# Optimization experiments

Measured on AMD Instinct MI355X. Metric: run time of the kernel, lower is better.

The kernel has to match this reference:

```python
import jax, jax.numpy as jnp
import numpy as np

SCORE_THR = 0.05
IOU_THR = 0.5
MAX_PER_IMG = 100
PRE_NMS_K = 2048  # fixed candidate budget for jit-compatible NMS
NUM_CLASSES = 80
MEANS = jnp.array([0.0, 0.0, 0.0, 0.0], jnp.float32)
STDS = jnp.array([0.1, 0.1, 0.2, 0.2], jnp.float32)
WH_RATIO_CLIP = 16.0 / 1000.0


def setup_inputs() -> dict:
    key = jax.random.key(0)
    B, N, C = 4, 8192, NUM_CLASSES
    H, W = 800, 1333
    k1, k2, k3, k4, k5, k6 = jax.random.split(key, 6)
    class_outs = jax.random.normal(k1, (B * N, C + 1), jnp.float32)
    regression_outs = jax.random.normal(k2, (B * N, C * 4), jnp.float32) * 0.5
    x1 = jax.random.uniform(k3, (B, N), minval=0.0, maxval=W * 0.8)
    y1 = jax.random.uniform(k4, (B, N), minval=0.0, maxval=H * 0.8)
    w = jax.random.uniform(k5, (B, N), minval=8.0, maxval=W * 0.2)
    h = jax.random.uniform(k6, (B, N), minval=8.0, maxval=H * 0.2)
    boxes = jnp.stack([x1, y1, jnp.minimum(x1 + w, float(W)), jnp.minimum(y1 + h, float(H))], axis=-1)
    return {"class_outs": class_outs, "regression_outs": regression_outs, "boxes": boxes, "img_h": H, "img_w": W}


def delta2bbox(proposals, deltas, H, W):
    # proposals [N,4], deltas [N, C*4] -> decoded boxes [N, C, 4]
    d = deltas.reshape(deltas.shape[0], -1, 4) * STDS + MEANS
    dx, dy, dw, dh = d[..., 0], d[..., 1], d[..., 2], d[..., 3]
    max_ratio = jnp.abs(jnp.log(jnp.float32(WH_RATIO_CLIP)))
    dw = jnp.clip(dw, -max_ratio, max_ratio)
    dh = jnp.clip(dh, -max_ratio, max_ratio)
    px = (proposals[:, 0] + proposals[:, 2]) * 0.5
    py = (proposals[:, 1] + proposals[:, 3]) * 0.5
    pw = proposals[:, 2] - proposals[:, 0]
    ph = proposals[:, 3] - proposals[:, 1]
    gx = px[:, None] + pw[:, None] * dx
    gy = py[:, None] + ph[:, None] * dy
    gw = pw[:, None] * jnp.exp(dw)
    gh = ph[:, None] * jnp.exp(dh)
    x1 = jnp.clip(gx - gw * 0.5, 0.0, float(W))
    y1 = jnp.clip(gy - gh * 0.5, 0.0, float(H))
    x2 = jnp.clip(gx + gw * 0.5, 0.0, float(W))
    y2 = jnp.clip(gy + gh * 0.5, 0.0, float(H))
    return jnp.stack([x1, y1, x2, y2], axis=-1)


def pairwise_iou(b):
    # b [K,4] -> [K,K]
    area = jnp.maximum(b[:, 2] - b[:, 0], 0.0) * jnp.maximum(b[:, 3] - b[:, 1], 0.0)
    lt = jnp.maximum(b[:, None, :2], b[None, :, :2])
    rb = jnp.minimum(b[:, None, 2:], b[None, :, 2:])
    wh = jnp.clip(rb - lt, 0.0)
    inter = wh[..., 0] * wh[..., 1]
    union = area[:, None] + area[None, :] - inter
    return inter / jnp.maximum(union, 1e-6)


def per_image(cls_out, reg_out, props, H, W):
    C = NUM_CLASSES
    scores = jax.nn.softmax(cls_out, axis=-1)[:, :C]        # drop background column
    bboxes = delta2bbox(props[:, :4], reg_out, H, W)        # [N, C, 4]
    flat_s = scores.reshape(-1)                             # [N*C]
    flat_s = jnp.where(flat_s > SCORE_THR, flat_s, -1.0)
    top_s, top_i = jax.lax.top_k(flat_s, PRE_NMS_K)
    cand = bboxes.reshape(-1, 4)[top_i]                     # [K,4]
    labels = top_i % C
    valid = top_s > 0.0
    # class-aware NMS via coordinate offsets per class
    offset = labels.astype(cand.dtype)[:, None] * (float(max(H, W)) + 1.0)
    iou = pairwise_iou(cand + offset)                       # [K,K]
    idx = jnp.arange(PRE_NMS_K)

    def body(i, keep):
        sup = (iou[i] > IOU_THR) & (idx > i) & keep[i]
        return keep & ~sup

    keep = jax.lax.fori_loop(0, PRE_NMS_K, body, valid)
    fs = jnp.where(keep, top_s, -1.0)
    out_s, order = jax.lax.top_k(fs, MAX_PER_IMG)
    ok = out_s > 0.0
    det_boxes = jnp.where(ok[:, None], cand[order], 0.0)
    det_scores = jnp.where(ok, out_s, 0.0)
    det_labels = jnp.where(ok, labels[order], -1)
    det_inds = jnp.where(ok, top_i[order], -1)
    return det_boxes, det_scores, det_labels, det_inds


def reference(class_outs, regression_outs, boxes, img_h, img_w):
    B, N = boxes.shape[:2]
    cls = class_outs.reshape(B, N, -1)
    reg = regression_outs.reshape(B, N, -1)
    f = jax.vmap(lambda c, r, p: per_image(c, r, p, img_h, img_w))
    det_boxes, det_scores, det_labels, det_inds = f(cls, reg, boxes)
    return det_boxes, det_scores, det_labels, det_inds
```

## Files before the change

### kernel.cpp

```cpp
#include <hip/hip_runtime.h>
#include <cstdint>
#include <cstddef>

#pragma clang fp contract(off)

typedef unsigned long long u64;
typedef unsigned int u32;

#define B_IMG 4
#define N_ROI 8192
#define NCLS 80
#define NCOL 81
#define K_NMS 2048
#define MAXOUT 100
#define THR_SCORE 0.05f
#define THR_IOU 0.5f

#define NBIN 4096
#define BIN_OFF 62771u
#define NSEG 16
#define GSEGCAP 4096
#define STGN 4096

__global__ __launch_bounds__(256) void k_zero(u32* __restrict__ p, int nwords) {
  int i = blockIdx.x * 256 + threadIdx.x;
  if (i < nwords) p[i] = 0;
}

__device__ __forceinline__ void softmax_row(const float* __restrict__ row, int lane,
                                            float& s0, float& s1) {
  float v0 = row[lane];
  float v1 = (lane < NCOL - 64) ? row[64 + lane] : -1e38f;
  float m = fmaxf(v0, v1);
  for (int o = 32; o; o >>= 1) m = fmaxf(m, __shfl_xor(m, o));
  float e0 = expf(v0 - m);
  float e1 = (lane < NCOL - 64) ? expf(v1 - m) : 0.0f;
  float s = e0 + e1;
  for (int o = 32; o; o >>= 1) s += __shfl_xor(s, o);
  s0 = e0 / s;
  s1 = e1 / s;
}

__global__ __launch_bounds__(1024) void k_hist(const float* __restrict__ cls,
                                               u32* __restrict__ hist,
                                               u32* __restrict__ gcnt,
                                               u64* __restrict__ glist) {
#pragma clang fp contract(off)
  __shared__ u32 lh[NBIN];
  __shared__ u32 wbase[16];
  __shared__ u32 blkcnt;
  __shared__ u32 gbase;
  int t = threadIdx.x, wv = t >> 6, lane = t & 63;
  for (int i = t; i < NBIN; i += 1024) lh[i] = 0;
  if (t == 0) blkcnt = 0;
  __syncthreads();

  int wid = blockIdx.x * 16 + wv;
  int b = wid >> 13;
  int n = wid & (N_ROI - 1);

  float s0, s1;
  softmax_row(cls + (size_t)wid * NCOL, lane, s0, s1);
  bool c0 = s0 > THR_SCORE;
  bool c1 = (lane < 16) && (s1 > THR_SCORE);
  if (c0) atomicAdd(&lh[(__float_as_uint(s0) >> 14) - BIN_OFF], 1u);
  if (c1) atomicAdd(&lh[(__float_as_uint(s1) >> 14) - BIN_OFF], 1u);

  u64 b0 = __ballot(c0), b1 = __ballot(c1);
  int cnt = __popcll(b0) + __popcll(b1);
  if (lane == 0) wbase[wv] = atomicAdd(&blkcnt, (u32)cnt);
  __syncthreads();

  int seg = blockIdx.x & (NSEG - 1);
  if (t == 0) gbase = atomicAdd(&gcnt[b * NSEG + seg], blkcnt);

  u32* gh = hist + (size_t)b * NBIN;
  for (int i = t; i < NBIN; i += 1024) {
    u32 c = lh[i];
    if (c) atomicAdd(&gh[i], c);
  }
  __syncthreads();

  u32 base = gbase + wbase[wv];
  u64 lm = (1ull << lane) - 1ull;
  u64* seglist = glist + ((size_t)(b * NSEG + seg)) * GSEGCAP;
  if (c0) {
    u32 pos = base + (u32)__popcll(b0 & lm);
    if (pos < GSEGCAP) {
      u32 flat = (u32)(n * NCLS + lane);
      seglist[pos] = ((u64)__float_as_uint(s0) << 32) | (u32)(~flat);
    }
  }
  if (c1) {
    u32 pos = base + (u32)__popcll(b0) + (u32)__popcll(b1 & lm);
    if (pos < GSEGCAP) {
      u32 flat = (u32)(n * NCLS + 64 + lane);
      seglist[pos] = ((u64)__float_as_uint(s1) << 32) | (u32)(~flat);
    }
  }
}

__global__ __launch_bounds__(1024) void k_cutbase(const u32* __restrict__ hist,
                                                  u32* __restrict__ cutg,
                                                  u32* __restrict__ binbase,
                                                  u32* __restrict__ bincnt,
                                                  u32* __restrict__ keptT) {
  __shared__ u32 wsum[16];
  __shared__ int best;
  __shared__ u32 cutsh;
  int b = blockIdx.x, t = threadIdx.x;
  int lane = t & 63, wv = t >> 6;
  const u32* gh = hist + (size_t)b * NBIN;
  u32 v0 = gh[t * 4 + 0], v1 = gh[t * 4 + 1], v2 = gh[t * 4 + 2], v3 = gh[t * 4 + 3];
  u32 my = v0 + v1 + v2 + v3;
  u32 inc = my;
  for (int o = 1; o < 64; o <<= 1) {
    u32 x = __shfl_up(inc, o);
    if (lane >= o) inc += x;
  }
  if (lane == 63) wsum[wv] = inc;
  if (t == 0) best = 0;

  u32* bc = bincnt + (size_t)b * NBIN + t * 4;
  bc[0] = 0; bc[1] = 0; bc[2] = 0; bc[3] = 0;
  __syncthreads();

  u32 wpre = 0;
  for (int i = 0; i < wv; ++i) wpre += wsum[i];
  u32 total = 0;
  for (int i = 0; i < 16; ++i) total += wsum[i];
  u32 excl = wpre + (inc - my);

  u32* bb = binbase + (size_t)b * NBIN + t * 4;
  u32 pi = excl;
  pi += v0; bb[0] = total - pi;
  pi += v1; bb[1] = total - pi;
  pi += v2; bb[2] = total - pi;
  pi += v3; bb[3] = total - pi;

  if (total >= K_NMS) {
    u32 lim = total - K_NMS;
    u32 p = excl;
    int cand = -1;
    if (p <= lim) cand = t * 4 + 0; p += v0;
    if (p <= lim) cand = t * 4 + 1; p += v1;
    if (p <= lim) cand = t * 4 + 2; p += v2;
    if (p <= lim) cand = t * 4 + 3; p += v3;
    if (cand >= 0) atomicMax(&best, cand);
  }
  __syncthreads();
  if (t == 0) {
    u32 c = (total >= K_NMS) ? (u32)best : 0u;
    cutsh = c;
    cutg[b] = c;
  }
  __syncthreads();
  u32 c = cutsh;
  if (t == (int)(c >> 2)) {
    u32 pe = excl;
    int r = (int)(c & 3);
    if (r > 0) pe += v0;
    if (r > 1) pe += v1;
    if (r > 2) pe += v2;
    keptT[b] = total - pe;
  }
}

__global__ __launch_bounds__(256) void k_scatter(const u32* __restrict__ gcnt,
                                                 const u64* __restrict__ glist,
                                                 const u32* __restrict__ cutg,
                                                 const u32* __restrict__ binbase,
                                                 u32* __restrict__ bincnt,
                                                 u64* __restrict__ staging) {
  int sid = blockIdx.x;
  int b = sid >> 4;
  u32 c = cutg[b];
  u32 m = gcnt[sid];
  if (m > GSEGCAP) m = GSEGCAP;
  const u64* sl = glist + (size_t)sid * GSEGCAP;
  for (u32 i = threadIdx.x; i < m; i += 256) {
    u64 key = sl[i];
    u32 bin = (u32)(key >> 46) - BIN_OFF;
    if (bin >= c) {
      u32 slot = binbase[(size_t)b * NBIN + bin] +
                 atomicAdd(&bincnt[(size_t)b * NBIN + bin], 1u);
      if (slot < STGN) staging[(size_t)b * STGN + slot] = key;
    }
  }
}

__global__ __launch_bounds__(256) void k_rankdecode(const u32* __restrict__ keptT,
                                                    const u32* __restrict__ binbase,
                                                    const u32* __restrict__ bincnt,
                                                    const u64* __restrict__ staging,
                                                    const float* __restrict__ props,
                                                    const float* __restrict__ regs,
                                                    const int* __restrict__ pH,
                                                    const int* __restrict__ pW,
                                                    float4* __restrict__ raw4,
                                                    float4* __restrict__ off4,
                                                    float* __restrict__ area,
                                                    float* __restrict__ scoref,
                                                    int* __restrict__ labeli,
                                                    int* __restrict__ flati) {
#pragma clang fp contract(off)
  int p0 = blockIdx.x * 256 + threadIdx.x;
  int b = p0 >> 12;
  int i = p0 & (STGN - 1);
  u32 T = keptT[b];
  if (T > STGN) T = STGN;

  if ((u32)i >= T) {
    if ((u32)i < K_NMS) {
      size_t g = (size_t)b * K_NMS + i;
      raw4[g] = make_float4(0.f, 0.f, 0.f, 0.f);
      off4[g] = make_float4(0.f, 0.f, 0.f, 0.f);
      area[g] = 0.f; scoref[g] = -1.0f; labeli[g] = 0; flati[g] = 0;
    }
    return;
  }

  u64 key = staging[(size_t)b * STGN + i];
  u32 bin = (u32)(key >> 46) - BIN_OFF;
  u32 base = binbase[(size_t)b * NBIN + bin];
  u32 cnt = bincnt[(size_t)b * NBIN + bin];
  u32 end = base + cnt;
  if (end > STGN) end = STGN;
  u32 rank = 0;
  for (u32 j = base; j < end; ++j)
    rank += (staging[(size_t)b * STGN + j] > key) ? 1u : 0u;
  u32 gslot = base + rank;
  if (gslot >= K_NMS) return;
  size_t g = (size_t)b * K_NMS + gslot;

  float Hf = (float)pH[0];
  float Wf = (float)pW[0];
  float offc = fmaxf(Hf, Wf) + 1.0f;

  u32 flat = ~(u32)(key & 0xFFFFFFFFull);
  float sc = __uint_as_float((u32)(key >> 32));
  int n = (int)(flat / NCLS);
  int c = (int)(flat - (u32)n * NCLS);

  float4 p = ((const float4*)props)[b * N_ROI + n];
  const float4 dl = *(const float4*)(regs + ((size_t)(b * N_ROI + n)) * (NCLS * 4) + c * 4);

  float mr = fabsf(logf(16.0f / 1000.0f));
  float dx = dl.x * 0.1f;
  float dy = dl.y * 0.1f;
  float dw = fminf(fmaxf(dl.z * 0.2f, -mr), mr);
  float dh = fminf(fmaxf(dl.w * 0.2f, -mr), mr);

  float px = (p.x + p.z) * 0.5f;
  float py = (p.y + p.w) * 0.5f;
  float pw = p.z - p.x;
  float ph = p.w - p.y;

  float tx = pw * dx; float gx = px + tx;
  float ty = ph * dy; float gy = py + ty;
  float gw = pw * expf(dw);
  float gh = ph * expf(dh);
  float hx = gw * 0.5f, hy = gh * 0.5f;

  float x1 = fminf(fmaxf(gx - hx, 0.0f), Wf);
  float y1 = fminf(fmaxf(gy - hy, 0.0f), Hf);
  float x2 = fminf(fmaxf(gx + hx, 0.0f), Wf);
  float y2 = fminf(fmaxf(gy + hy, 0.0f), Hf);

  raw4[g] = make_float4(x1, y1, x2, y2);

  float off = (float)c * offc;
  float ox1 = x1 + off, oy1 = y1 + off, ox2 = x2 + off, oy2 = y2 + off;
  off4[g] = make_float4(ox1, oy1, ox2, oy2);
  area[g] = fmaxf(ox2 - ox1, 0.0f) * fmaxf(oy2 - oy1, 0.0f);
  scoref[g] = sc;
  labeli[g] = c;
  flati[g] = (int)flat;
}

__global__ __launch_bounds__(256) void k_mask(const float4* __restrict__ off4,
                                              const float* __restrict__ area,
                                              u64* __restrict__ masks) {
#pragma clang fp contract(off)
  int wave = threadIdx.x >> 6, lane = threadIdx.x & 63;
  int R = blockIdx.x * 4 + wave;
  int b = R >> 11, i = R & (K_NMS - 1);
  const float4* bb = off4 + (size_t)b * K_NMS;
  const float* aa = area + (size_t)b * K_NMS;
  float4 bi = bb[i];
  float ai = aa[i];
  u64 my = 0;
  for (int w = i >> 6; w < 32; ++w) {
    int j = (w << 6) + lane;
    float4 bj = bb[j];
    float lx = fmaxf(bi.x, bj.x);
    float ly = fmaxf(bi.y, bj.y);
    float rx = fminf(bi.z, bj.z);
    float ry = fminf(bi.w, bj.w);
    float ww = fmaxf(rx - lx, 0.0f);
    float hh = fmaxf(ry - ly, 0.0f);
    float inter = ww * hh;
    float uni = (ai + aa[j]) - inter;
    float iou = inter / fmaxf(uni, 1e-6f);
    bool sup = (j > i) && (iou > THR_IOU);
    u64 word = __ballot(sup);
    if (lane == w) my = word;
  }
  if (lane < 32) masks[((size_t)R << 5) + lane] = my;
}

__global__ __launch_bounds__(64, 1) void k_scanout(const u64* __restrict__ masks,
                                                   const u32* __restrict__ keptT,
                                                   const float* __restrict__ scoref,
                                                   const float4* __restrict__ raw4,
                                                   const int* __restrict__ labeli,
                                                   const int* __restrict__ flati,
                                                   float* __restrict__ out) {
  int b = blockIdx.x;
  int lane = threadIdx.x;

  u32 Tc = keptT[b];
  if (Tc > K_NMS) Tc = K_NMS;
  u64 kw = 0;
  if (lane < 32) {
    int rem = (int)Tc - (lane << 6);
    kw = (rem >= 64) ? ~0ull : ((rem > 0) ? ((1ull << rem) - 1ull) : 0ull);
  }

  const u64* mrow = masks + ((size_t)b << 16);
  int myw = lane & 31;
  int half = lane >> 5;

  u64 dnext = mrow[((size_t)lane << 5) + 0];

  for (int c = 0; c < 32; ++c) {
    u64 dcur = dnext;
    if (c < 31) dnext = mrow[((size_t)((c + 1) * 64 + lane) << 5) + (c + 1)];

    const u64* rb = mrow + (((size_t)(c * 64 + half * 32)) << 5) + myw;
    u64 r0 = rb[0u << 5],  r1 = rb[1u << 5],  r2 = rb[2u << 5],  r3 = rb[3u << 5];
    u64 r4 = rb[4u << 5],  r5 = rb[5u << 5],  r6 = rb[6u << 5],  r7 = rb[7u << 5];
    u64 r8 = rb[8u << 5],  r9 = rb[9u << 5],  r10 = rb[10u << 5], r11 = rb[11u << 5];
    u64 r12 = rb[12u << 5], r13 = rb[13u << 5], r14 = rb[14u << 5], r15 = rb[15u << 5];
    u64 r16 = rb[16u << 5], r17 = rb[17u << 5], r18 = rb[18u << 5], r19 = rb[19u << 5];
    u64 r20 = rb[20u << 5], r21 = rb[21u << 5], r22 = rb[22u << 5], r23 = rb[23u << 5];
    u64 r24 = rb[24u << 5], r25 = rb[25u << 5], r26 = rb[26u << 5], r27 = rb[27u << 5];
    u64 r28 = rb[28u << 5], r29 = rb[29u << 5], r30 = rb[30u << 5], r31 = rb[31u << 5];
    asm volatile("" : "+v"(r0), "+v"(r1), "+v"(r2), "+v"(r3));
    asm volatile("" : "+v"(r4), "+v"(r5), "+v"(r6), "+v"(r7));
    asm volatile("" : "+v"(r8), "+v"(r9), "+v"(r10), "+v"(r11));
    asm volatile("" : "+v"(r12), "+v"(r13), "+v"(r14), "+v"(r15));
    asm volatile("" : "+v"(r16), "+v"(r17), "+v"(r18), "+v"(r19));
    asm volatile("" : "+v"(r20), "+v"(r21), "+v"(r22), "+v"(r23));
    asm volatile("" : "+v"(r24), "+v"(r25), "+v"(r26), "+v"(r27));
    asm volatile("" : "+v"(r28), "+v"(r29), "+v"(r30), "+v"(r31));

    u32 dlo = (u32)dcur, dhi = (u32)(dcur >> 32);
    u64 kc = ((u64)(u32)__builtin_amdgcn_readlane((int)(u32)(kw >> 32), c) << 32) |
             (u32)__builtin_amdgcn_readlane((int)(u32)kw, c);
#pragma unroll
    for (int d = 0; d < 64; ++d) {
      u64 dg = ((u64)(u32)__builtin_amdgcn_readlane((int)dhi, d) << 32) |
               (u32)__builtin_amdgcn_readlane((int)dlo, d);
      u64 on = (u64)0 - ((kc >> d) & 1ull);
      kc &= ~(dg & on);
    }

    u32 kb = half ? (u32)(kc >> 32) : (u32)kc;
#define ONB(r) ((u64)0 - (u64)((kb >> (r)) & 1u))
    u64 a0 = (r0 & ONB(0)) | (r1 & ONB(1)) | (r2 & ONB(2)) | (r3 & ONB(3)) |
             (r4 & ONB(4)) | (r5 & ONB(5)) | (r6 & ONB(6)) | (r7 & ONB(7));
    u64 a1 = (r8 & ONB(8)) | (r9 & ONB(9)) | (r10 & ONB(10)) | (r11 & ONB(11)) |
             (r12 & ONB(12)) | (r13 & ONB(13)) | (r14 & ONB(14)) | (r15 & ONB(15));
    u64 a2 = (r16 & ONB(16)) | (r17 & ONB(17)) | (r18 & ONB(18)) | (r19 & ONB(19)) |
             (r20 & ONB(20)) | (r21 & ONB(21)) | (r22 & ONB(22)) | (r23 & ONB(23));
    u64 a3 = (r24 & ONB(24)) | (r25 & ONB(25)) | (r26 & ONB(26)) | (r27 & ONB(27)) |
             (r28 & ONB(28)) | (r29 & ONB(29)) | (r30 & ONB(30)) | (r31 & ONB(31));
#undef ONB
    u64 supp = (a0 | a1) | (a2 | a3);
    supp |= __shfl_xor(supp, 32);
    kw &= ~supp;

    int fin = (lane <= c) ? __popcll(kw) : 0;
    for (int o = 32; o; o >>= 1) fin += __shfl_xor(fin, o);
    if (fin >= MAXOUT) break;
  }

  int pc = (lane < 32) ? __popcll(kw) : 0;
  int pre = pc;
  for (int o = 1; o < 64; o <<= 1) {
    int v = __shfl_up(pre, o);
    if (lane >= o) pre += v;
  }
  int excl = pre - pc;
  int total = __shfl(pre, 63);

  float* ob = out;
  float* os = out + B_IMG * MAXOUT * 4;
  float* ol = os + B_IMG * MAXOUT;
  float* oi = ol + B_IMG * MAXOUT;

  if (lane < 32) {
    u64 w = kw;
    int r = excl;
    while (w) {
      int bit = __ffsll((long long)w) - 1;
      w &= w - 1;
      if (r < MAXOUT) {
        int j = (lane << 6) + bit;
        size_t g = (size_t)b * K_NMS + j;
        float4 bx = raw4[g];
        int o = b * MAXOUT + r;
        ob[o * 4 + 0] = bx.x; ob[o * 4 + 1] = bx.y;
        ob[o * 4 + 2] = bx.z; ob[o * 4 + 3] = bx.w;
        os[o] = scoref[g];
        ol[o] = (float)labeli[g];
        oi[o] = (float)flati[g];
      }
      ++r;
    }
  }
  for (int r = total + lane; r < MAXOUT; r += 64) {
    int o = b * MAXOUT + r;
    ob[o * 4 + 0] = 0.f; ob[o * 4 + 1] = 0.f; ob[o * 4 + 2] = 0.f; ob[o * 4 + 3] = 0.f;
    os[o] = 0.f;
    ol[o] = -1.0f;
    oi[o] = -1.0f;
  }
}

extern "C" void kernel_launch(void* const* d_in, const int* in_sizes, int n_in,
                              void* d_out, int out_size, void* d_ws, size_t ws_size,
                              hipStream_t stream) {
  const float* cls = (const float*)d_in[0];
  const float* regs = (const float*)d_in[1];
  const float* props = (const float*)d_in[2];
  const int* pH = (const int*)d_in[3];
  const int* pW = (const int*)d_in[4];

  char* ws = (char*)d_ws;
  size_t o = 0;
  u32* hist = (u32*)(ws + o); o += (size_t)B_IMG * NBIN * sizeof(u32);
  u32* gcnt = (u32*)(ws + o); o += (size_t)B_IMG * NSEG * sizeof(u32);
  int zero_words = (int)(o / sizeof(u32));
  u32* bincnt = (u32*)(ws + o); o += (size_t)B_IMG * NBIN * sizeof(u32);
  u32* cutg = (u32*)(ws + o); o += 256;
  u32* keptT = (u32*)(ws + o); o += 256;
  u32* binbase = (u32*)(ws + o); o += (size_t)B_IMG * NBIN * sizeof(u32);
  u64* glist = (u64*)(ws + o); o += (size_t)B_IMG * NSEG * GSEGCAP * sizeof(u64);
  u64* staging = (u64*)(ws + o); o += (size_t)B_IMG * STGN * sizeof(u64);
  float4* raw4 = (float4*)(ws + o); o += (size_t)B_IMG * K_NMS * sizeof(float4);
  float4* off4 = (float4*)(ws + o); o += (size_t)B_IMG * K_NMS * sizeof(float4);
  float* area = (float*)(ws + o); o += (size_t)B_IMG * K_NMS * sizeof(float);
  float* scoref = (float*)(ws + o); o += (size_t)B_IMG * K_NMS * sizeof(float);
  int* labeli = (int*)(ws + o); o += (size_t)B_IMG * K_NMS * sizeof(int);
  int* flati = (int*)(ws + o); o += (size_t)B_IMG * K_NMS * sizeof(int);
  u64* masks = (u64*)(ws + o); o += (size_t)B_IMG * K_NMS * 32 * sizeof(u64);

  k_zero<<<(zero_words + 255) / 256, 256, 0, stream>>>(hist, zero_words);
  k_hist<<<B_IMG * N_ROI / 16, 1024, 0, stream>>>(cls, hist, gcnt, glist);
  k_cutbase<<<B_IMG, 1024, 0, stream>>>(hist, cutg, binbase, bincnt, keptT);
  k_scatter<<<B_IMG * NSEG, 256, 0, stream>>>(gcnt, glist, cutg, binbase, bincnt, staging);
  k_rankdecode<<<B_IMG * STGN / 256, 256, 0, stream>>>(keptT, binbase, bincnt, staging,
                                                       props, regs, pH, pW,
                                                       raw4, off4, area, scoref, labeli, flati);
  k_mask<<<B_IMG * K_NMS / 4, 256, 0, stream>>>(off4, area, masks);
  k_scanout<<<B_IMG, 64, 0, stream>>>(masks, keptT, scoref, raw4, labeli, flati, (float*)d_out);
}
```

Baseline: 84.01 us.

## Fuse histogram, cut, scatter and rank-decode into one per-image select kernel

Replaces the zero/hist/cutbase/scatter/rankdecode chain with two kernels. A score kernel writes per-block candidate lists and counts without global atomics, and a single 1024-thread block per image builds the histogram, cut, scatter and decode in shared memory. This removes three launches, the zeroing pass and global atomic traffic. In exchange the decode and rank stage now runs on only 4 blocks, which serialises work that used to be spread across many blocks, and it needs large shared-memory staging.

After: 93.63 us. +11.5%, slower.

```diff
diff --git a/kernel.cpp b/kernel.cpp
--- a/kernel.cpp
+++ b/kernel.cpp
@@ -18,14 +18,9 @@
 
 #define NBIN 4096
 #define BIN_OFF 62771u
-#define NSEG 16
-#define GSEGCAP 4096
+#define RPI 2048
+#define BLKCAP 128
 #define STGN 4096
-
-__global__ __launch_bounds__(256) void k_zero(u32* __restrict__ p, int nwords) {
-  int i = blockIdx.x * 256 + threadIdx.x;
-  if (i < nwords) p[i] = 0;
-}
 
 __device__ __forceinline__ void softmax_row(const float* __restrict__ row, int lane,
                                             float& s0, float& s1) {
@@ -41,106 +36,126 @@
   s1 = e1 / s;
 }
 
-__global__ __launch_bounds__(1024) void k_hist(const float* __restrict__ cls,
-                                               u32* __restrict__ hist,
-                                               u32* __restrict__ gcnt,
+__global__ __launch_bounds__(256) void k_score(const float* __restrict__ cls,
+                                               u32* __restrict__ blkcnt,
                                                u64* __restrict__ glist) {
 #pragma clang fp contract(off)
-  __shared__ u32 lh[NBIN];
-  __shared__ u32 wbase[16];
-  __shared__ u32 blkcnt;
-  __shared__ u32 gbase;
+  __shared__ u32 wcnt[4];
   int t = threadIdx.x, wv = t >> 6, lane = t & 63;
-  for (int i = t; i < NBIN; i += 1024) lh[i] = 0;
-  if (t == 0) blkcnt = 0;
-  __syncthreads();
-
-  int wid = blockIdx.x * 16 + wv;
-  int b = wid >> 13;
+  int wid = blockIdx.x * 4 + wv;
   int n = wid & (N_ROI - 1);
 
   float s0, s1;
   softmax_row(cls + (size_t)wid * NCOL, lane, s0, s1);
   bool c0 = s0 > THR_SCORE;
   bool c1 = (lane < 16) && (s1 > THR_SCORE);
-  if (c0) atomicAdd(&lh[(__float_as_uint(s0) >> 14) - BIN_OFF], 1u);
-  if (c1) atomicAdd(&lh[(__float_as_uint(s1) >> 14) - BIN_OFF], 1u);
-
   u64 b0 = __ballot(c0), b1 = __ballot(c1);
   int cnt = __popcll(b0) + __popcll(b1);
-  if (lane == 0) wbase[wv] = atomicAdd(&blkcnt, (u32)cnt);
-  __syncthreads();
-
-  int seg = blockIdx.x & (NSEG - 1);
-  if (t == 0) gbase = atomicAdd(&gcnt[b * NSEG + seg], blkcnt);
-
-  u32* gh = hist + (size_t)b * NBIN;
-  for (int i = t; i < NBIN; i += 1024) {
-    u32 c = lh[i];
-    if (c) atomicAdd(&gh[i], c);
-  }
-  __syncthreads();
-
-  u32 base = gbase + wbase[wv];
+  if (lane == 0) wcnt[wv] = (u32)cnt;
+  __syncthreads();
+  u32 wbase = 0;
+  for (int i = 0; i < wv; ++i) wbase += wcnt[i];
+  if (t == 0) blkcnt[blockIdx.x] = wcnt[0] + wcnt[1] + wcnt[2] + wcnt[3];
+
   u64 lm = (1ull << lane) - 1ull;
-  u64* seglist = glist + ((size_t)(b * NSEG + seg)) * GSEGCAP;
+  u64* reg = glist + (size_t)blockIdx.x * BLKCAP;
   if (c0) {
-    u32 pos = base + (u32)__popcll(b0 & lm);
-    if (pos < GSEGCAP) {
+    u32 pos = wbase + (u32)__popcll(b0 & lm);
+    if (pos < BLKCAP) {
       u32 flat = (u32)(n * NCLS + lane);
-      seglist[pos] = ((u64)__float_as_uint(s0) << 32) | (u32)(~flat);
+      reg[pos] = ((u64)__float_as_uint(s0) << 32) | (u32)(~flat);
     }
   }
   if (c1) {
-    u32 pos = base + (u32)__popcll(b0) + (u32)__popcll(b1 & lm);
-    if (pos < GSEGCAP) {
+    u32 pos = wbase + (u32)__popcll(b0) + (u32)__popcll(b1 & lm);
+    if (pos < BLKCAP) {
       u32 flat = (u32)(n * NCLS + 64 + lane);
-      seglist[pos] = ((u64)__float_as_uint(s1) << 32) | (u32)(~flat);
-    }
-  }
-}
-
-__global__ __launch_bounds__(1024) void k_cutbase(const u32* __restrict__ hist,
-                                                  u32* __restrict__ cutg,
-                                                  u32* __restrict__ binbase,
-                                                  u32* __restrict__ bincnt,
-                                                  u32* __restrict__ keptT) {
+      reg[pos] = ((u64)__float_as_uint(s1) << 32) | (u32)(~flat);
+    }
+  }
+}
+
+__global__ __launch_bounds__(1024) void k_select(const u32* __restrict__ blkcnt,
+                                                 const u64* __restrict__ glist,
+                                                 const float* __restrict__ props,
+                                                 const float* __restrict__ regs,
+                                                 const int* __restrict__ pH,
+                                                 const int* __restrict__ pW,
+                                                 u32* __restrict__ keptTg,
+                                                 float4* __restrict__ raw4,
+                                                 float4* __restrict__ off4,
+                                                 float* __restrict__ area,
+                                                 float* __restrict__ scoref,
+                                                 int* __restrict__ labeli,
+                                                 int* __restrict__ flati) {
+#pragma clang fp contract(off)
+  __shared__ u32 pref[RPI + 1];
+  __shared__ u32 lh[NBIN];
+  __shared__ u32 bbase[NBIN];
+  __shared__ u32 bcnt[NBIN];
+  __shared__ u64 stg[STGN];
   __shared__ u32 wsum[16];
   __shared__ int best;
   __shared__ u32 cutsh;
   int b = blockIdx.x, t = threadIdx.x;
   int lane = t & 63, wv = t >> 6;
-  const u32* gh = hist + (size_t)b * NBIN;
-  u32 v0 = gh[t * 4 + 0], v1 = gh[t * 4 + 1], v2 = gh[t * 4 + 2], v3 = gh[t * 4 + 3];
-  u32 my = v0 + v1 + v2 + v3;
+
+  u32 rc0 = blkcnt[b * RPI + t * 2];
+  u32 rc1 = blkcnt[b * RPI + t * 2 + 1];
+  if (rc0 > BLKCAP) rc0 = BLKCAP;
+  if (rc1 > BLKCAP) rc1 = BLKCAP;
+  u32 my = rc0 + rc1;
   u32 inc = my;
   for (int o = 1; o < 64; o <<= 1) {
     u32 x = __shfl_up(inc, o);
     if (lane >= o) inc += x;
   }
   if (lane == 63) wsum[wv] = inc;
+  for (int i = t; i < NBIN; i += 1024) { lh[i] = 0; bcnt[i] = 0; }
   if (t == 0) best = 0;
-
-  u32* bc = bincnt + (size_t)b * NBIN + t * 4;
-  bc[0] = 0; bc[1] = 0; bc[2] = 0; bc[3] = 0;
-  __syncthreads();
-
+  __syncthreads();
   u32 wpre = 0;
   for (int i = 0; i < wv; ++i) wpre += wsum[i];
-  u32 total = 0;
-  for (int i = 0; i < 16; ++i) total += wsum[i];
-  u32 excl = wpre + (inc - my);
-
-  u32* bb = binbase + (size_t)b * NBIN + t * 4;
-  u32 pi = excl;
-  pi += v0; bb[0] = total - pi;
-  pi += v1; bb[1] = total - pi;
-  pi += v2; bb[2] = total - pi;
-  pi += v3; bb[3] = total - pi;
-
-  if (total >= K_NMS) {
-    u32 lim = total - K_NMS;
-    u32 p = excl;
+  u32 T = 0;
+  for (int i = 0; i < 16; ++i) T += wsum[i];
+  u32 excl = wpre + inc - my;
+  pref[t * 2] = excl;
+  pref[t * 2 + 1] = excl + rc0;
+  if (t == 0) pref[RPI] = T;
+  __syncthreads();
+
+  const u64* gbase = glist + (size_t)b * RPI * BLKCAP;
+  for (u32 i = t; i < T; i += 1024) {
+    u32 lo = 0, hi = RPI;
+    while (hi - lo > 1) { u32 mid = (lo + hi) >> 1; if (pref[mid] <= i) lo = mid; else hi = mid; }
+    u64 key = gbase[(size_t)lo * BLKCAP + (i - pref[lo])];
+    atomicAdd(&lh[(u32)(key >> 46) - BIN_OFF], 1u);
+  }
+  __syncthreads();
+
+  u32 v0 = lh[t * 4 + 0], v1 = lh[t * 4 + 1], v2 = lh[t * 4 + 2], v3 = lh[t * 4 + 3];
+  u32 myh = v0 + v1 + v2 + v3;
+  u32 inch = myh;
+  for (int o = 1; o < 64; o <<= 1) {
+    u32 x = __shfl_up(inch, o);
+    if (lane >= o) inch += x;
+  }
+  __syncthreads();
+  if (lane == 63) wsum[wv] = inch;
+  __syncthreads();
+  u32 wpreh = 0;
+  for (int i = 0; i < wv; ++i) wpreh += wsum[i];
+  u32 toth = 0;
+  for (int i = 0; i < 16; ++i) toth += wsum[i];
+  u32 exclh = wpreh + inch - myh;
+  u32 pi = exclh;
+  pi += v0; bbase[t * 4 + 0] = toth - pi;
+  pi += v1; bbase[t * 4 + 1] = toth - pi;
+  pi += v2; bbase[t * 4 + 2] = toth - pi;
+  pi += v3; bbase[t * 4 + 3] = toth - pi;
+  if (toth >= K_NMS) {
+    u32 lim = toth - K_NMS;
+    u32 p = exclh;
     int cand = -1;
     if (p <= lim) cand = t * 4 + 0; p += v0;
     if (p <= lim) cand = t * 4 + 1; p += v1;
@@ -149,133 +164,103 @@
     if (cand >= 0) atomicMax(&best, cand);
   }
   __syncthreads();
-  if (t == 0) {
-    u32 c = (total >= K_NMS) ? (u32)best : 0u;
-    cutsh = c;
-    cutg[b] = c;
-  }
-  __syncthreads();
-  u32 c = cutsh;
-  if (t == (int)(c >> 2)) {
-    u32 pe = excl;
-    int r = (int)(c & 3);
+  if (t == 0) cutsh = (toth >= K_NMS) ? (u32)best : 0u;
+  __syncthreads();
+  u32 cut = cutsh;
+  if (t == (int)(cut >> 2)) {
+    u32 pe = exclh;
+    int r = (int)(cut & 3);
     if (r > 0) pe += v0;
     if (r > 1) pe += v1;
     if (r > 2) pe += v2;
-    keptT[b] = total - pe;
-  }
-}
-
-__global__ __launch_bounds__(256) void k_scatter(const u32* __restrict__ gcnt,
-                                                 const u64* __restrict__ glist,
-                                                 const u32* __restrict__ cutg,
-                                                 const u32* __restrict__ binbase,
-                                                 u32* __restrict__ bincnt,
-                                                 u64* __restrict__ staging) {
-  int sid = blockIdx.x;
-  int b = sid >> 4;
-  u32 c = cutg[b];
-  u32 m = gcnt[sid];
-  if (m > GSEGCAP) m = GSEGCAP;
-  const u64* sl = glist + (size_t)sid * GSEGCAP;
-  for (u32 i = threadIdx.x; i < m; i += 256) {
-    u64 key = sl[i];
+    u32 kept = toth - pe;
+    wsum[0] = kept;
+    keptTg[b] = kept;
+  }
+  __syncthreads();
+  u32 keptv = wsum[0];
+
+  for (u32 i = t; i < T; i += 1024) {
+    u32 lo = 0, hi = RPI;
+    while (hi - lo > 1) { u32 mid = (lo + hi) >> 1; if (pref[mid] <= i) lo = mid; else hi = mid; }
+    u64 key = gbase[(size_t)lo * BLKCAP + (i - pref[lo])];
     u32 bin = (u32)(key >> 46) - BIN_OFF;
-    if (bin >= c) {
-      u32 slot = binbase[(size_t)b * NBIN + bin] +
-                 atomicAdd(&bincnt[(size_t)b * NBIN + bin], 1u);
-      if (slot < STGN) staging[(size_t)b * STGN + slot] = key;
-    }
-  }
-}
-
-__global__ __launch_bounds__(256) void k_rankdecode(const u32* __restrict__ keptT,
-                                                    const u32* __restrict__ binbase,
-                                                    const u32* __restrict__ bincnt,
-                                                    const u64* __restrict__ staging,
-                                                    const float* __restrict__ props,
-                                                    const float* __restrict__ regs,
-                                                    const int* __restrict__ pH,
-                                                    const int* __restrict__ pW,
-                                                    float4* __restrict__ raw4,
-                                                    float4* __restrict__ off4,
-                                                    float* __restrict__ area,
-                                                    float* __restrict__ scoref,
-                                                    int* __restrict__ labeli,
-                                                    int* __restrict__ flati) {
-#pragma clang fp contract(off)
-  int p0 = blockIdx.x * 256 + threadIdx.x;
-  int b = p0 >> 12;
-  int i = p0 & (STGN - 1);
-  u32 T = keptT[b];
-  if (T > STGN) T = STGN;
-
-  if ((u32)i >= T) {
-    if ((u32)i < K_NMS) {
-      size_t g = (size_t)b * K_NMS + i;
-      raw4[g] = make_float4(0.f, 0.f, 0.f, 0.f);
-      off4[g] = make_float4(0.f, 0.f, 0.f, 0.f);
-      area[g] = 0.f; scoref[g] = -1.0f; labeli[g] = 0; flati[g] = 0;
-    }
-    return;
-  }
-
-  u64 key = staging[(size_t)b * STGN + i];
-  u32 bin = (u32)(key >> 46) - BIN_OFF;
-  u32 base = binbase[(size_t)b * NBIN + bin];
-  u32 cnt = bincnt[(size_t)b * NBIN + bin];
-  u32 end = base + cnt;
-  if (end > STGN) end = STGN;
-  u32 rank = 0;
-  for (u32 j = base; j < end; ++j)
-    rank += (staging[(size_t)b * STGN + j] > key) ? 1u : 0u;
-  u32 gslot = base + rank;
-  if (gslot >= K_NMS) return;
-  size_t g = (size_t)b * K_NMS + gslot;
-
+    if (bin >= cut) {
+      u32 slot = bbase[bin] + atomicAdd(&bcnt[bin], 1u);
+      if (slot < STGN) stg[slot] = key;
+    }
+  }
+  __syncthreads();
+
+  u32 Tk = keptv;
+  if (Tk > STGN) Tk = STGN;
   float Hf = (float)pH[0];
   float Wf = (float)pW[0];
   float offc = fmaxf(Hf, Wf) + 1.0f;
-
-  u32 flat = ~(u32)(key & 0xFFFFFFFFull);
-  float sc = __uint_as_float((u32)(key >> 32));
-  int n = (int)(flat / NCLS);
-  int c = (int)(flat - (u32)n * NCLS);
-
-  float4 p = ((const float4*)props)[b * N_ROI + n];
-  const float4 dl = *(const float4*)(regs + ((size_t)(b * N_ROI + n)) * (NCLS * 4) + c * 4);
-
   float mr = fabsf(logf(16.0f / 1000.0f));
-  float dx = dl.x * 0.1f;
-  float dy = dl.y * 0.1f;
-  float dw = fminf(fmaxf(dl.z * 0.2f, -mr), mr);
-  float dh = fminf(fmaxf(dl.w * 0.2f, -mr), mr);
-
-  float px = (p.x + p.z) * 0.5f;
-  float py = (p.y + p.w) * 0.5f;
-  float pw = p.z - p.x;
-  float ph = p.w - p.y;
-
-  float tx = pw * dx; float gx = px + tx;
-  float ty = ph * dy; float gy = py + ty;
-  float gw = pw * expf(dw);
-  float gh = ph * expf(dh);
-  float hx = gw * 0.5f, hy = gh * 0.5f;
-
-  float x1 = fminf(fmaxf(gx - hx, 0.0f), Wf);
-  float y1 = fminf(fmaxf(gy - hy, 0.0f), Hf);
-  float x2 = fminf(fmaxf(gx + hx, 0.0f), Wf);
-  float y2 = fminf(fmaxf(gy + hy, 0.0f), Hf);
-
-  raw4[g] = make_float4(x1, y1, x2, y2);
-
-  float off = (float)c * offc;
-  float ox1 = x1 + off, oy1 = y1 + off, ox2 = x2 + off, oy2 = y2 + off;
-  off4[g] = make_float4(ox1, oy1, ox2, oy2);
-  area[g] = fmaxf(ox2 - ox1, 0.0f) * fmaxf(oy2 - oy1, 0.0f);
-  scoref[g] = sc;
-  labeli[g] = c;
-  flati[g] = (int)flat;
+
+  for (u32 i = t; i < STGN; i += 1024) {
+    if (i >= Tk) {
+      if (i < K_NMS) {
+        size_t g = (size_t)b * K_NMS + i;
+        raw4[g] = make_float4(0.f, 0.f, 0.f, 0.f);
+        off4[g] = make_float4(0.f, 0.f, 0.f, 0.f);
+        area[g] = 0.f; scoref[g] = -1.0f; labeli[g] = 0; flati[g] = 0;
+      }
+      continue;
+    }
+    u64 key = stg[i];
+    u32 bin = (u32)(key >> 46) - BIN_OFF;
+    u32 base = bbase[bin];
+    u32 cnt = bcnt[bin];
+    u32 end = base + cnt;
+    if (end > STGN) end = STGN;
+    u32 rank = 0;
+    for (u32 j = base; j < end; ++j)
+      rank += (stg[j] > key) ? 1u : 0u;
+    u32 gslot = base + rank;
+    if (gslot >= K_NMS) continue;
+    size_t g = (size_t)b * K_NMS + gslot;
+
+    u32 flat = ~(u32)(key & 0xFFFFFFFFull);
+    float sc = __uint_as_float((u32)(key >> 32));
+    int n = (int)(flat / NCLS);
+    int c = (int)(flat - (u32)n * NCLS);
+
+    float4 p = ((const float4*)props)[b * N_ROI + n];
+    const float4 dl = *(const float4*)(regs + ((size_t)(b * N_ROI + n)) * (NCLS * 4) + c * 4);
+
+    float dx = dl.x * 0.1f;
+    float dy = dl.y * 0.1f;
+    float dw = fminf(fmaxf(dl.z * 0.2f, -mr), mr);
+    float dh = fminf(fmaxf(dl.w * 0.2f, -mr), mr);
+
+    float px = (p.x + p.z) * 0.5f;
+    float py = (p.y + p.w) * 0.5f;
+    float pw = p.z - p.x;
+    float ph = p.w - p.y;
+
+    float tx = pw * dx; float gx = px + tx;
+    float ty = ph * dy; float gy = py + ty;
+    float gw = pw * expf(dw);
+    float gh2 = ph * expf(dh);
+    float hx = gw * 0.5f, hy = gh2 * 0.5f;
+
+    float x1 = fminf(fmaxf(gx - hx, 0.0f), Wf);
+    float y1 = fminf(fmaxf(gy - hy, 0.0f), Hf);
+    float x2 = fminf(fmaxf(gx + hx, 0.0f), Wf);
+    float y2 = fminf(fmaxf(gy + hy, 0.0f), Hf);
+
+    raw4[g] = make_float4(x1, y1, x2, y2);
+
+    float off = (float)c * offc;
+    float ox1 = x1 + off, oy1 = y1 + off, ox2 = x2 + off, oy2 = y2 + off;
+    off4[g] = make_float4(ox1, oy1, ox2, oy2);
+    area[g] = fmaxf(ox2 - ox1, 0.0f) * fmaxf(oy2 - oy1, 0.0f);
+    scoref[g] = sc;
+    labeli[g] = c;
+    flati[g] = (int)flat;
+  }
 }
 
 __global__ __launch_bounds__(256) void k_mask(const float4* __restrict__ off4,
@@ -440,15 +425,9 @@
 
   char* ws = (char*)d_ws;
   size_t o = 0;
-  u32* hist = (u32*)(ws + o); o += (size_t)B_IMG * NBIN * sizeof(u32);
-  u32* gcnt = (u32*)(ws + o); o += (size_t)B_IMG * NSEG * sizeof(u32);
-  int zero_words = (int)(o / sizeof(u32));
-  u32* bincnt = (u32*)(ws + o); o += (size_t)B_IMG * NBIN * sizeof(u32);
-  u32* cutg = (u32*)(ws + o); o += 256;
+  u32* blkcnt = (u32*)(ws + o); o += (size_t)B_IMG * RPI * sizeof(u32);
   u32* keptT = (u32*)(ws + o); o += 256;
-  u32* binbase = (u32*)(ws + o); o += (size_t)B_IMG * NBIN * sizeof(u32);
-  u64* glist = (u64*)(ws + o); o += (size_t)B_IMG * NSEG * GSEGCAP * sizeof(u64);
-  u64* staging = (u64*)(ws + o); o += (size_t)B_IMG * STGN * sizeof(u64);
+  u64* glist = (u64*)(ws + o); o += (size_t)B_IMG * RPI * BLKCAP * sizeof(u64);
   float4* raw4 = (float4*)(ws + o); o += (size_t)B_IMG * K_NMS * sizeof(float4);
   float4* off4 = (float4*)(ws + o); o += (size_t)B_IMG * K_NMS * sizeof(float4);
   float* area = (float*)(ws + o); o += (size_t)B_IMG * K_NMS * sizeof(float);
@@ -457,13 +436,9 @@
   int* flati = (int*)(ws + o); o += (size_t)B_IMG * K_NMS * sizeof(int);
   u64* masks = (u64*)(ws + o); o += (size_t)B_IMG * K_NMS * 32 * sizeof(u64);
 
-  k_zero<<<(zero_words + 255) / 256, 256, 0, stream>>>(hist, zero_words);
-  k_hist<<<B_IMG * N_ROI / 16, 1024, 0, stream>>>(cls, hist, gcnt, glist);
-  k_cutbase<<<B_IMG, 1024, 0, stream>>>(hist, cutg, binbase, bincnt, keptT);
-  k_scatter<<<B_IMG * NSEG, 256, 0, stream>>>(gcnt, glist, cutg, binbase, bincnt, staging);
-  k_rankdecode<<<B_IMG * STGN / 256, 256, 0, stream>>>(keptT, binbase, bincnt, staging,
-                                                       props, regs, pH, pW,
-                                                       raw4, off4, area, scoref, labeli, flati);
+  k_score<<<B_IMG * RPI, 256, 0, stream>>>(cls, blkcnt, glist);
+  k_select<<<B_IMG, 1024, 0, stream>>>(blkcnt, glist, props, regs, pH, pW, keptT,
+                                       raw4, off4, area, scoref, labeli, flati);
   k_mask<<<B_IMG * K_NMS / 4, 256, 0, stream>>>(off4, area, masks);
   k_scanout<<<B_IMG, 64, 0, stream>>>(masks, keptT, scoref, raw4, labeli, flati, (float*)d_out);
 }
```

## Replace global histogram atomics with per-block candidate regions and deferred histogram

Applied to the files above, without the earlier changes.

The scoring kernel now writes each block's candidates into a fixed 128-slot region and records a per-block count. It no longer builds a 4096-bin shared histogram per block and merges it into global memory with atomics. A new per-image kernel builds the histogram from those regions and computes the cut, which also removes the separate zeroing launch. The scatter kernel walks the padded per-block regions. The risk is that a block producing more than 128 candidates would drop entries, and the histogram pass is done serially by only four blocks.

After: 75.78 us. -9.8%, faster.

```diff
diff --git a/kernel.cpp b/kernel.cpp
--- a/kernel.cpp
+++ b/kernel.cpp
@@ -18,14 +18,9 @@
 
 #define NBIN 4096
 #define BIN_OFF 62771u
-#define NSEG 16
-#define GSEGCAP 4096
+#define RPI 2048
+#define BLKCAP 128
 #define STGN 4096
-
-__global__ __launch_bounds__(256) void k_zero(u32* __restrict__ p, int nwords) {
-  int i = blockIdx.x * 256 + threadIdx.x;
-  if (i < nwords) p[i] = 0;
-}
 
 __device__ __forceinline__ void softmax_row(const float* __restrict__ row, int lane,
                                             float& s0, float& s1) {
@@ -41,77 +36,74 @@
   s1 = e1 / s;
 }
 
-__global__ __launch_bounds__(1024) void k_hist(const float* __restrict__ cls,
-                                               u32* __restrict__ hist,
-                                               u32* __restrict__ gcnt,
+__global__ __launch_bounds__(256) void k_score(const float* __restrict__ cls,
+                                               u32* __restrict__ blkcnt,
                                                u64* __restrict__ glist) {
 #pragma clang fp contract(off)
-  __shared__ u32 lh[NBIN];
-  __shared__ u32 wbase[16];
-  __shared__ u32 blkcnt;
-  __shared__ u32 gbase;
+  __shared__ u32 wcnt[4];
   int t = threadIdx.x, wv = t >> 6, lane = t & 63;
-  for (int i = t; i < NBIN; i += 1024) lh[i] = 0;
-  if (t == 0) blkcnt = 0;
-  __syncthreads();
-
-  int wid = blockIdx.x * 16 + wv;
-  int b = wid >> 13;
+  int wid = blockIdx.x * 4 + wv;
   int n = wid & (N_ROI - 1);
 
   float s0, s1;
   softmax_row(cls + (size_t)wid * NCOL, lane, s0, s1);
   bool c0 = s0 > THR_SCORE;
   bool c1 = (lane < 16) && (s1 > THR_SCORE);
-  if (c0) atomicAdd(&lh[(__float_as_uint(s0) >> 14) - BIN_OFF], 1u);
-  if (c1) atomicAdd(&lh[(__float_as_uint(s1) >> 14) - BIN_OFF], 1u);
-
   u64 b0 = __ballot(c0), b1 = __ballot(c1);
   int cnt = __popcll(b0) + __popcll(b1);
-  if (lane == 0) wbase[wv] = atomicAdd(&blkcnt, (u32)cnt);
-  __syncthreads();
-
-  int seg = blockIdx.x & (NSEG - 1);
-  if (t == 0) gbase = atomicAdd(&gcnt[b * NSEG + seg], blkcnt);
-
-  u32* gh = hist + (size_t)b * NBIN;
-  for (int i = t; i < NBIN; i += 1024) {
-    u32 c = lh[i];
-    if (c) atomicAdd(&gh[i], c);
-  }
-  __syncthreads();
-
-  u32 base = gbase + wbase[wv];
+  if (lane == 0) wcnt[wv] = (u32)cnt;
+  __syncthreads();
+  u32 wbase = 0;
+  for (int i = 0; i < wv; ++i) wbase += wcnt[i];
+  if (t == 0) blkcnt[blockIdx.x] = wcnt[0] + wcnt[1] + wcnt[2] + wcnt[3];
+
   u64 lm = (1ull << lane) - 1ull;
-  u64* seglist = glist + ((size_t)(b * NSEG + seg)) * GSEGCAP;
+  u64* reg = glist + (size_t)blockIdx.x * BLKCAP;
   if (c0) {
-    u32 pos = base + (u32)__popcll(b0 & lm);
-    if (pos < GSEGCAP) {
+    u32 pos = wbase + (u32)__popcll(b0 & lm);
+    if (pos < BLKCAP) {
       u32 flat = (u32)(n * NCLS + lane);
-      seglist[pos] = ((u64)__float_as_uint(s0) << 32) | (u32)(~flat);
+      reg[pos] = ((u64)__float_as_uint(s0) << 32) | (u32)(~flat);
     }
   }
   if (c1) {
-    u32 pos = base + (u32)__popcll(b0) + (u32)__popcll(b1 & lm);
-    if (pos < GSEGCAP) {
+    u32 pos = wbase + (u32)__popcll(b0) + (u32)__popcll(b1 & lm);
+    if (pos < BLKCAP) {
       u32 flat = (u32)(n * NCLS + 64 + lane);
-      seglist[pos] = ((u64)__float_as_uint(s1) << 32) | (u32)(~flat);
-    }
-  }
-}
-
-__global__ __launch_bounds__(1024) void k_cutbase(const u32* __restrict__ hist,
+      reg[pos] = ((u64)__float_as_uint(s1) << 32) | (u32)(~flat);
+    }
+  }
+}
+
+__global__ __launch_bounds__(1024) void k_histcut(const u32* __restrict__ blkcnt,
+                                                  const u64* __restrict__ glist,
                                                   u32* __restrict__ cutg,
                                                   u32* __restrict__ binbase,
                                                   u32* __restrict__ bincnt,
                                                   u32* __restrict__ keptT) {
+  __shared__ u32 lh[NBIN];
   __shared__ u32 wsum[16];
   __shared__ int best;
   __shared__ u32 cutsh;
   int b = blockIdx.x, t = threadIdx.x;
   int lane = t & 63, wv = t >> 6;
-  const u32* gh = hist + (size_t)b * NBIN;
-  u32 v0 = gh[t * 4 + 0], v1 = gh[t * 4 + 1], v2 = gh[t * 4 + 2], v3 = gh[t * 4 + 3];
+
+  for (int i = t; i < NBIN; i += 1024) lh[i] = 0;
+  __syncthreads();
+
+  for (int r = t; r < RPI; r += 1024) {
+    u32 cnt = blkcnt[b * RPI + r];
+    if (cnt > BLKCAP) cnt = BLKCAP;
+    const u64* reg = glist + ((size_t)(b * RPI + r)) * BLKCAP;
+    for (u32 k = 0; k < cnt; ++k) {
+      u64 key = reg[k];
+      atomicAdd(&lh[(u32)(key >> 46) - BIN_OFF], 1u);
+    }
+  }
+  if (t == 0) best = 0;
+  __syncthreads();
+
+  u32 v0 = lh[t * 4 + 0], v1 = lh[t * 4 + 1], v2 = lh[t * 4 + 2], v3 = lh[t * 4 + 3];
   u32 my = v0 + v1 + v2 + v3;
   u32 inc = my;
   for (int o = 1; o < 64; o <<= 1) {
@@ -119,7 +111,6 @@
     if (lane >= o) inc += x;
   }
   if (lane == 63) wsum[wv] = inc;
-  if (t == 0) best = 0;
 
   u32* bc = bincnt + (size_t)b * NBIN + t * 4;
   bc[0] = 0; bc[1] = 0; bc[2] = 0; bc[3] = 0;
@@ -166,25 +157,34 @@
   }
 }
 
-__global__ __launch_bounds__(256) void k_scatter(const u32* __restrict__ gcnt,
+__global__ __launch_bounds__(256) void k_scatter(const u32* __restrict__ blkcnt,
                                                  const u64* __restrict__ glist,
                                                  const u32* __restrict__ cutg,
                                                  const u32* __restrict__ binbase,
                                                  u32* __restrict__ bincnt,
                                                  u64* __restrict__ staging) {
-  int sid = blockIdx.x;
-  int b = sid >> 4;
-  u32 c = cutg[b];
-  u32 m = gcnt[sid];
-  if (m > GSEGCAP) m = GSEGCAP;
-  const u64* sl = glist + (size_t)sid * GSEGCAP;
-  for (u32 i = threadIdx.x; i < m; i += 256) {
-    u64 key = sl[i];
-    u32 bin = (u32)(key >> 46) - BIN_OFF;
-    if (bin >= c) {
-      u32 slot = binbase[(size_t)b * NBIN + bin] +
-                 atomicAdd(&bincnt[(size_t)b * NBIN + bin], 1u);
-      if (slot < STGN) staging[(size_t)b * STGN + slot] = key;
+  __shared__ u32 lcnt[32];
+  int blk = blockIdx.x;
+  int b = blk >> 6;
+  int r0 = (blk & 63) * 32;
+  int t = threadIdx.x;
+  if (t < 32) {
+    u32 cc = blkcnt[b * RPI + r0 + t];
+    lcnt[t] = (cc > BLKCAP) ? BLKCAP : cc;
+  }
+  __syncthreads();
+  u32 cut = cutg[b];
+  for (int idx = t; idx < 32 * BLKCAP; idx += 256) {
+    int r = idx >> 7;
+    int k = idx & (BLKCAP - 1);
+    if ((u32)k < lcnt[r]) {
+      u64 key = glist[((size_t)(b * RPI + r0 + r)) * BLKCAP + k];
+      u32 bin = (u32)(key >> 46) - BIN_OFF;
+      if (bin >= cut) {
+        u32 slot = binbase[(size_t)b * NBIN + bin] +
+                   atomicAdd(&bincnt[(size_t)b * NBIN + bin], 1u);
+        if (slot < STGN) staging[(size_t)b * STGN + slot] = key;
+      }
     }
   }
 }
@@ -440,14 +440,12 @@
 
   char* ws = (char*)d_ws;
   size_t o = 0;
-  u32* hist = (u32*)(ws + o); o += (size_t)B_IMG * NBIN * sizeof(u32);
-  u32* gcnt = (u32*)(ws + o); o += (size_t)B_IMG * NSEG * sizeof(u32);
-  int zero_words = (int)(o / sizeof(u32));
+  u32* blkcnt = (u32*)(ws + o); o += (size_t)B_IMG * RPI * sizeof(u32);
+  u32* keptT = (u32*)(ws + o); o += 256;
+  u32* cutg = (u32*)(ws + o); o += 256;
+  u32* binbase = (u32*)(ws + o); o += (size_t)B_IMG * NBIN * sizeof(u32);
   u32* bincnt = (u32*)(ws + o); o += (size_t)B_IMG * NBIN * sizeof(u32);
-  u32* cutg = (u32*)(ws + o); o += 256;
-  u32* keptT = (u32*)(ws + o); o += 256;
-  u32* binbase = (u32*)(ws + o); o += (size_t)B_IMG * NBIN * sizeof(u32);
-  u64* glist = (u64*)(ws + o); o += (size_t)B_IMG * NSEG * GSEGCAP * sizeof(u64);
+  u64* glist = (u64*)(ws + o); o += (size_t)B_IMG * RPI * BLKCAP * sizeof(u64);
   u64* staging = (u64*)(ws + o); o += (size_t)B_IMG * STGN * sizeof(u64);
   float4* raw4 = (float4*)(ws + o); o += (size_t)B_IMG * K_NMS * sizeof(float4);
   float4* off4 = (float4*)(ws + o); o += (size_t)B_IMG * K_NMS * sizeof(float4);
@@ -457,10 +455,9 @@
   int* flati = (int*)(ws + o); o += (size_t)B_IMG * K_NMS * sizeof(int);
   u64* masks = (u64*)(ws + o); o += (size_t)B_IMG * K_NMS * 32 * sizeof(u64);
 
-  k_zero<<<(zero_words + 255) / 256, 256, 0, stream>>>(hist, zero_words);
-  k_hist<<<B_IMG * N_ROI / 16, 1024, 0, stream>>>(cls, hist, gcnt, glist);
-  k_cutbase<<<B_IMG, 1024, 0, stream>>>(hist, cutg, binbase, bincnt, keptT);
-  k_scatter<<<B_IMG * NSEG, 256, 0, stream>>>(gcnt, glist, cutg, binbase, bincnt, staging);
+  k_score<<<B_IMG * RPI, 256, 0, stream>>>(cls, blkcnt, glist);
+  k_histcut<<<B_IMG, 1024, 0, stream>>>(blkcnt, glist, cutg, binbase, bincnt, keptT);
+  k_scatter<<<256, 256, 0, stream>>>(blkcnt, glist, cutg, binbase, bincnt, staging);
   k_rankdecode<<<B_IMG * STGN / 256, 256, 0, stream>>>(keptT, binbase, bincnt, staging,
                                                        props, regs, pH, pW,
                                                        raw4, off4, area, scoref, labeli, flati);
```
